# Performance work log

Hardware: AMD Instinct MI355X
Metric: run time of the kernel (lower is better)

Reference implementation:

```python
import jax, jax.numpy as jnp
import numpy as np


def setup_inputs() -> dict:
    key = jax.random.key(0)
    k1, k2 = jax.random.split(key)
    inputs = jax.random.normal(k1, (16, 64, 64, 512), dtype=jnp.float32)
    gamma = jax.random.normal(k2, (1,), dtype=jnp.float32)
    return {"inputs": inputs, "gamma": gamma}


def reference(inputs, gamma):
    # inputs: [B, H, W, C] (NHWC), gamma: [1]
    b, h, w, c = inputs.shape
    vec_a = inputs.reshape(b, h * w, c)           # [B, HW, C]
    # channel-channel Gram matrix: [B, C, C]
    aTa = jnp.einsum('bnc,bnd->bcd', vec_a, vec_a)
    softmax_aTa = jax.nn.softmax(aTa, axis=-1)     # softmax over last channel axis
    # attend over channels: [B, HW, C] @ [B, C, C] -> [B, HW, C]
    aaTa = jnp.einsum('bnc,bcd->bnd', vec_a, softmax_aTa)
    aaTa = aaTa.reshape(b, h, w, c)
    return gamma * aaTa + inputs
```

## Files before the change

kernel.cpp:

```cpp
#include <hip/hip_runtime.h>
#include <stdint.h>

#define BB 16
#define NN 4096
#define CC 512

typedef __attribute__((ext_vector_type(8))) short bf16x8;
typedef __attribute__((ext_vector_type(4))) float f32x4;

__device__ __forceinline__ unsigned short to_bf16(float f) {
  unsigned int u = __float_as_uint(f);
  u += 0x7fffu + ((u >> 16) & 1u);
  return (unsigned short)(u >> 16);
}

__device__ __forceinline__ void gload_lds16(const void* g, void* l) {
  __builtin_amdgcn_global_load_lds(
      (const __attribute__((address_space(1))) unsigned int*)g,
      (__attribute__((address_space(3))) unsigned int*)l, 16, 0, 0);
}

template <int KT>
__device__ __forceinline__ void nt_gemm(const unsigned short* __restrict__ aB,
                                        const unsigned short* __restrict__ bB,
                                        f32x4 acc[4][4],
                                        unsigned short* lA, unsigned short* lB) {
  const int tid  = threadIdx.x;
  const int wid  = tid >> 6;
  const int lane = tid & 63;
  const int wr   = (wid >> 1) * 64;
  const int wc   = (wid & 1) * 64;

  const f32x4 zero = {0.f, 0.f, 0.f, 0.f};
#pragma unroll
  for (int i = 0; i < 4; ++i)
#pragma unroll
    for (int j = 0; j < 4; ++j) acc[i][j] = zero;

  const int srow = lane >> 3;
  const int gsrc = (lane & 7) ^ srow;

#pragma unroll 1
  for (int k0 = 0; k0 < KT; k0 += 64) {
#pragma unroll
    for (int i = 0; i < 4; ++i) {
      const int issue = wid * 4 + i;
      const int row   = issue * 8 + srow;
      const size_t go = (size_t)row * KT + k0 + gsrc * 8;
      gload_lds16(aB + go, lA + issue * 512);
      gload_lds16(bB + go, lB + issue * 512);
    }
    __syncthreads();

#pragma unroll
    for (int s = 0; s < 2; ++s) {
      bf16x8 af[4], bfr[4];
#pragma unroll
      for (int mf = 0; mf < 4; ++mf) {
        const int row = wr + mf * 16 + (lane & 15);
        const int ch  = (s * 4 + (lane >> 4)) ^ (row & 7);
        af[mf] = *(const bf16x8*)(lA + row * 64 + ch * 8);
      }
#pragma unroll
      for (int nf = 0; nf < 4; ++nf) {
        const int row = wc + nf * 16 + (lane & 15);
        const int ch  = (s * 4 + (lane >> 4)) ^ (row & 7);
        bfr[nf] = *(const bf16x8*)(lB + row * 64 + ch * 8);
      }
#pragma unroll
      for (int mf = 0; mf < 4; ++mf)
#pragma unroll
        for (int nf = 0; nf < 4; ++nf)
          acc[mf][nf] = __builtin_amdgcn_mfma_f32_16x16x32_bf16(
              af[mf], bfr[nf], acc[mf][nf], 0, 0, 0);
    }
    __syncthreads();
  }
}

__global__ __launch_bounds__(256) void k_convert(const float* __restrict__ in,
                                                 unsigned short* __restrict__ a16,
                                                 unsigned short* __restrict__ at16) {
  __shared__ unsigned short lt[64][68];
  const int b  = blockIdx.y;
  const int tn = blockIdx.x >> 3, tc = blockIdx.x & 7;
  const int n0 = tn * 64, c0 = tc * 64;
  const float* src = in + ((size_t)b * NN + n0) * CC + c0;
  unsigned short* adst = a16 + ((size_t)b * NN + n0) * CC + c0;

#pragma unroll
  for (int i = 0; i < 4; ++i) {
    const int id = i * 256 + threadIdx.x;
    const int n = id >> 4, ch = id & 15;
    float4 v = *(const float4*)(src + (size_t)n * CC + ch * 4);
    ushort4 o;
    o.x = to_bf16(v.x); o.y = to_bf16(v.y); o.z = to_bf16(v.z); o.w = to_bf16(v.w);
    *(ushort4*)(adst + (size_t)n * CC + ch * 4) = o;
    lt[ch * 4 + 0][n] = o.x;
    lt[ch * 4 + 1][n] = o.y;
    lt[ch * 4 + 2][n] = o.z;
    lt[ch * 4 + 3][n] = o.w;
  }
  __syncthreads();
  unsigned short* tdst = at16 + ((size_t)b * CC + c0) * NN + n0;
#pragma unroll
  for (int i = 0; i < 4; ++i) {
    const int id = i * 256 + threadIdx.x;
    const int c = id >> 4, ch2 = id & 15;
    uint2 w = *(const uint2*)&lt[c][ch2 * 4];
    *(uint2*)(tdst + (size_t)c * NN + ch2 * 4) = w;
  }
}

__global__ __launch_bounds__(256) void k_gram(const unsigned short* __restrict__ at,
                                              float* __restrict__ gram) {
  __shared__ __align__(16) unsigned short lA[128 * 64];
  __shared__ __align__(16) unsigned short lB[128 * 64];
  const int b  = blockIdx.y;
  const int c0 = (blockIdx.x & 3) * 128;
  const int d0 = (blockIdx.x >> 2) * 128;
  const unsigned short* aB = at + ((size_t)b * CC + c0) * NN;
  const unsigned short* bB = at + ((size_t)b * CC + d0) * NN;
  f32x4 acc[4][4];
  nt_gemm<NN>(aB, bB, acc, lA, lB);

  const int lane = threadIdx.x & 63, wid = threadIdx.x >> 6;
  const int wr = (wid >> 1) * 64, wc = (wid & 1) * 64;
  float* gb = gram + (size_t)b * CC * CC;
#pragma unroll
  for (int mf = 0; mf < 4; ++mf)
#pragma unroll
    for (int nf = 0; nf < 4; ++nf)
#pragma unroll
      for (int r = 0; r < 4; ++r) {
        const int row = c0 + wr + mf * 16 + (lane >> 4) * 4 + r;
        const int col = d0 + wc + nf * 16 + (lane & 15);
        gb[(size_t)row * CC + col] = acc[mf][nf][r];
      }
}

__global__ __launch_bounds__(256) void k_rowstats(const float* __restrict__ gram,
                                                  float2* __restrict__ stats) {
  const int wid = threadIdx.x >> 6, lane = threadIdx.x & 63;
  const int row = blockIdx.x * 4 + wid;
  const float* src = gram + (size_t)row * CC;
  float4 v0 = *(const float4*)(src + lane * 4);
  float4 v1 = *(const float4*)(src + 256 + lane * 4);
  float m = fmaxf(fmaxf(fmaxf(v0.x, v0.y), fmaxf(v0.z, v0.w)),
                  fmaxf(fmaxf(v1.x, v1.y), fmaxf(v1.z, v1.w)));
#pragma unroll
  for (int off = 32; off > 0; off >>= 1) m = fmaxf(m, __shfl_xor(m, off));
  float s = expf(v0.x - m) + expf(v0.y - m) + expf(v0.z - m) + expf(v0.w - m) +
            expf(v1.x - m) + expf(v1.y - m) + expf(v1.z - m) + expf(v1.w - m);
#pragma unroll
  for (int off = 32; off > 0; off >>= 1) s += __shfl_xor(s, off);
  if (lane == 0) stats[row] = make_float2(m, 1.0f / s);
}

__global__ __launch_bounds__(256) void k_smax_t(const float* __restrict__ gram,
                                                const float2* __restrict__ stats,
                                                unsigned short* __restrict__ st) {
  __shared__ unsigned short lt[64][68];
  const int b  = blockIdx.y;
  const int c0 = (blockIdx.x >> 3) * 64, d0 = (blockIdx.x & 7) * 64;
  const float* gb = gram + ((size_t)b * CC + c0) * CC + d0;
  const float2* sb = stats + (size_t)b * CC + c0;
#pragma unroll
  for (int i = 0; i < 4; ++i) {
    const int id = i * 256 + threadIdx.x;
    const int c = id >> 4, ch = id & 15;
    const float2 stt = sb[c];
    float4 v = *(const float4*)(gb + (size_t)c * CC + ch * 4);
    float vv[4] = {v.x, v.y, v.z, v.w};
#pragma unroll
    for (int j = 0; j < 4; ++j)
      lt[ch * 4 + j][c] = to_bf16(expf(vv[j] - stt.x) * stt.y);
  }
  __syncthreads();
  unsigned short* ob = st + ((size_t)b * CC + d0) * CC + c0;
#pragma unroll
  for (int i = 0; i < 4; ++i) {
    const int id = i * 256 + threadIdx.x;
    const int d = id >> 4, ch2 = id & 15;
    uint2 w = *(const uint2*)&lt[d][ch2 * 4];
    *(uint2*)(ob + (size_t)d * CC + ch2 * 4) = w;
  }
}

__global__ __launch_bounds__(256) void k_out(const unsigned short* __restrict__ a16,
                                             const unsigned short* __restrict__ st,
                                             const float* __restrict__ x,
                                             const float* __restrict__ gammap,
                                             float* __restrict__ outp) {
  __shared__ __align__(16) unsigned short lA[128 * 64];
  __shared__ __align__(16) unsigned short lB[128 * 64];
  const int b  = blockIdx.y;
  const int mt = blockIdx.x >> 2, nt = blockIdx.x & 3;
  const int n0 = mt * 128, d0 = nt * 128;
  const unsigned short* aB = a16 + ((size_t)b * NN + n0) * CC;
  const unsigned short* bB = st + ((size_t)b * CC + d0) * CC;
  f32x4 acc[4][4];
  nt_gemm<CC>(aB, bB, acc, lA, lB);

  const float g = gammap[0];
  const int lane = threadIdx.x & 63, wid = threadIdx.x >> 6;
  const int wr = (wid >> 1) * 64, wc = (wid & 1) * 64;
  const float* xb = x + ((size_t)b * NN + n0) * CC + d0;
  float* ob = outp + ((size_t)b * NN + n0) * CC + d0;
#pragma unroll
  for (int mf = 0; mf < 4; ++mf)
#pragma unroll
    for (int nf = 0; nf < 4; ++nf)
#pragma unroll
      for (int r = 0; r < 4; ++r) {
        const int row = wr + mf * 16 + (lane >> 4) * 4 + r;
        const int col = wc + nf * 16 + (lane & 15);
        const size_t off = (size_t)row * CC + col;
        ob[off] = fmaf(g, acc[mf][nf][r], xb[off]);
      }
}

extern "C" void kernel_launch(void* const* d_in, const int* in_sizes, int n_in,
                              void* d_out, int out_size, void* d_ws, size_t ws_size,
                              hipStream_t stream) {
  const float* in    = (const float*)d_in[0];
  const float* gamma = (const float*)d_in[1];
  float* outp = (float*)d_out;

  unsigned short* a16  = (unsigned short*)d_ws;
  float*          gram = (float*)((char*)d_ws + ((size_t)64 << 20));
  unsigned short* st   = (unsigned short*)((char*)d_ws + ((size_t)80 << 20));
  float2*         stats = (float2*)((char*)d_ws + ((size_t)88 << 20));
  unsigned short* at16 = (unsigned short*)d_out;

  k_convert<<<dim3(512, 16), 256, 0, stream>>>(in, a16, at16);
  k_gram<<<dim3(16, 16), 256, 0, stream>>>(at16, gram);
  k_rowstats<<<dim3(2048), 256, 0, stream>>>(gram, stats);
  k_smax_t<<<dim3(64, 16), 256, 0, stream>>>(gram, stats, st);
  k_out<<<dim3(128, 16), 256, 0, stream>>>(a16, st, in, gamma, outp);
}
```

Measured before the change: 403.4 us.

## Split-K Gram GEMM, fuse softmax stages, swizzle block order, read residual as bf16

New measurement: 370.7 us. 8.1% less time.

```diff
diff --git a/kernel.cpp b/kernel.cpp
--- a/kernel.cpp
+++ b/kernel.cpp
@@ -4,6 +4,7 @@
 #define BB 16
 #define NN 4096
 #define CC 512
+#define PELEM ((size_t)BB * CC * CC)
 
 typedef __attribute__((ext_vector_type(8))) short bf16x8;
 typedef __attribute__((ext_vector_type(4))) float f32x4;
@@ -13,6 +14,9 @@
   u += 0x7fffu + ((u >> 16) & 1u);
   return (unsigned short)(u >> 16);
 }
+__device__ __forceinline__ float bf16_to_f32(unsigned short h) {
+  return __uint_as_float(((unsigned int)h) << 16);
+}
 
 __device__ __forceinline__ void gload_lds16(const void* g, void* l) {
   __builtin_amdgcn_global_load_lds(
@@ -20,7 +24,7 @@
       (__attribute__((address_space(3))) unsigned int*)l, 16, 0, 0);
 }
 
-template <int KT>
+template <int RS, int KLEN>
 __device__ __forceinline__ void nt_gemm(const unsigned short* __restrict__ aB,
                                         const unsigned short* __restrict__ bB,
                                         f32x4 acc[4][4],
@@ -41,12 +45,12 @@
   const int gsrc = (lane & 7) ^ srow;
 
 #pragma unroll 1
-  for (int k0 = 0; k0 < KT; k0 += 64) {
+  for (int k0 = 0; k0 < KLEN; k0 += 64) {
 #pragma unroll
     for (int i = 0; i < 4; ++i) {
       const int issue = wid * 4 + i;
       const int row   = issue * 8 + srow;
-      const size_t go = (size_t)row * KT + k0 + gsrc * 8;
+      const size_t go = (size_t)row * RS + k0 + gsrc * 8;
       gload_lds16(aB + go, lA + issue * 512);
       gload_lds16(bB + go, lB + issue * 512);
     }
@@ -113,110 +117,134 @@
 }
 
 __global__ __launch_bounds__(256) void k_gram(const unsigned short* __restrict__ at,
-                                              float* __restrict__ gram) {
+                                              float* __restrict__ parts) {
   __shared__ __align__(16) unsigned short lA[128 * 64];
   __shared__ __align__(16) unsigned short lB[128 * 64];
-  const int b  = blockIdx.y;
-  const int c0 = (blockIdx.x & 3) * 128;
-  const int d0 = (blockIdx.x >> 2) * 128;
-  const unsigned short* aB = at + ((size_t)b * CC + c0) * NN;
-  const unsigned short* bB = at + ((size_t)b * CC + d0) * NN;
+  const int bid  = blockIdx.x;
+  const int work = (bid & 7) * 128 + (bid >> 3);
+  const int b    = work >> 6;
+  const int r    = work & 63;
+  const int ks   = r >> 4;
+  const int tile = r & 15;
+  const int c0 = (tile & 3) * 128;
+  const int d0 = (tile >> 2) * 128;
+  const unsigned short* aB = at + ((size_t)b * CC + c0) * NN + ks * 1024;
+  const unsigned short* bB = at + ((size_t)b * CC + d0) * NN + ks * 1024;
   f32x4 acc[4][4];
-  nt_gemm<NN>(aB, bB, acc, lA, lB);
+  nt_gemm<NN, 1024>(aB, bB, acc, lA, lB);
 
   const int lane = threadIdx.x & 63, wid = threadIdx.x >> 6;
   const int wr = (wid >> 1) * 64, wc = (wid & 1) * 64;
-  float* gb = gram + (size_t)b * CC * CC;
+  float* gb = parts + (size_t)ks * PELEM + (size_t)b * CC * CC;
 #pragma unroll
   for (int mf = 0; mf < 4; ++mf)
 #pragma unroll
     for (int nf = 0; nf < 4; ++nf)
 #pragma unroll
-      for (int r = 0; r < 4; ++r) {
-        const int row = c0 + wr + mf * 16 + (lane >> 4) * 4 + r;
+      for (int q = 0; q < 4; ++q) {
+        const int row = c0 + wr + mf * 16 + (lane >> 4) * 4 + q;
         const int col = d0 + wc + nf * 16 + (lane & 15);
-        gb[(size_t)row * CC + col] = acc[mf][nf][r];
-      }
-}
-
-__global__ __launch_bounds__(256) void k_rowstats(const float* __restrict__ gram,
-                                                  float2* __restrict__ stats) {
+        gb[(size_t)row * CC + col] = acc[mf][nf][q];
+      }
+}
+
+__global__ __launch_bounds__(256) void k_softmax(const float* __restrict__ parts,
+                                                 unsigned short* __restrict__ st) {
+  __shared__ unsigned short ls[32][512];
+  const int b  = blockIdx.x >> 4;
+  const int cb = blockIdx.x & 15;
   const int wid = threadIdx.x >> 6, lane = threadIdx.x & 63;
-  const int row = blockIdx.x * 4 + wid;
-  const float* src = gram + (size_t)row * CC;
-  float4 v0 = *(const float4*)(src + lane * 4);
-  float4 v1 = *(const float4*)(src + 256 + lane * 4);
-  float m = fmaxf(fmaxf(fmaxf(v0.x, v0.y), fmaxf(v0.z, v0.w)),
-                  fmaxf(fmaxf(v1.x, v1.y), fmaxf(v1.z, v1.w)));
-#pragma unroll
-  for (int off = 32; off > 0; off >>= 1) m = fmaxf(m, __shfl_xor(m, off));
-  float s = expf(v0.x - m) + expf(v0.y - m) + expf(v0.z - m) + expf(v0.w - m) +
-            expf(v1.x - m) + expf(v1.y - m) + expf(v1.z - m) + expf(v1.w - m);
-#pragma unroll
-  for (int off = 32; off > 0; off >>= 1) s += __shfl_xor(s, off);
-  if (lane == 0) stats[row] = make_float2(m, 1.0f / s);
-}
-
-__global__ __launch_bounds__(256) void k_smax_t(const float* __restrict__ gram,
-                                                const float2* __restrict__ stats,
-                                                unsigned short* __restrict__ st) {
-  __shared__ unsigned short lt[64][68];
-  const int b  = blockIdx.y;
-  const int c0 = (blockIdx.x >> 3) * 64, d0 = (blockIdx.x & 7) * 64;
-  const float* gb = gram + ((size_t)b * CC + c0) * CC + d0;
-  const float2* sb = stats + (size_t)b * CC + c0;
-#pragma unroll
-  for (int i = 0; i < 4; ++i) {
-    const int id = i * 256 + threadIdx.x;
-    const int c = id >> 4, ch = id & 15;
-    const float2 stt = sb[c];
-    float4 v = *(const float4*)(gb + (size_t)c * CC + ch * 4);
-    float vv[4] = {v.x, v.y, v.z, v.w};
-#pragma unroll
-    for (int j = 0; j < 4; ++j)
-      lt[ch * 4 + j][c] = to_bf16(expf(vv[j] - stt.x) * stt.y);
+
+#pragma unroll 1
+  for (int i = 0; i < 8; ++i) {
+    const int rl = wid * 8 + i;
+    const int c  = cb * 32 + rl;
+    const int r7 = rl & 7;
+    const float* base = parts + ((size_t)b * CC + c) * CC;
+    float4 v0 = {0.f, 0.f, 0.f, 0.f}, v1 = {0.f, 0.f, 0.f, 0.f};
+#pragma unroll
+    for (int p = 0; p < 4; ++p) {
+      float4 a = *(const float4*)(base + (size_t)p * PELEM + lane * 4);
+      float4 bq = *(const float4*)(base + (size_t)p * PELEM + 256 + lane * 4);
+      v0.x += a.x; v0.y += a.y; v0.z += a.z; v0.w += a.w;
+      v1.x += bq.x; v1.y += bq.y; v1.z += bq.z; v1.w += bq.w;
+    }
+    float m = fmaxf(fmaxf(fmaxf(v0.x, v0.y), fmaxf(v0.z, v0.w)),
+                    fmaxf(fmaxf(v1.x, v1.y), fmaxf(v1.z, v1.w)));
+#pragma unroll
+    for (int off = 32; off > 0; off >>= 1) m = fmaxf(m, __shfl_xor(m, off));
+    float e0 = expf(v0.x - m), e1 = expf(v0.y - m), e2 = expf(v0.z - m), e3 = expf(v0.w - m);
+    float e4 = expf(v1.x - m), e5 = expf(v1.y - m), e6 = expf(v1.z - m), e7 = expf(v1.w - m);
+    float s = e0 + e1 + e2 + e3 + e4 + e5 + e6 + e7;
+#pragma unroll
+    for (int off = 32; off > 0; off >>= 1) s += __shfl_xor(s, off);
+    const float pinv = 1.0f / s;
+    ushort4 o0, o1;
+    o0.x = to_bf16(e0 * pinv); o0.y = to_bf16(e1 * pinv);
+    o0.z = to_bf16(e2 * pinv); o0.w = to_bf16(e3 * pinv);
+    o1.x = to_bf16(e4 * pinv); o1.y = to_bf16(e5 * pinv);
+    o1.z = to_bf16(e6 * pinv); o1.w = to_bf16(e7 * pinv);
+    *(ushort4*)&ls[rl][(lane ^ r7) << 2]         = o0;
+    *(ushort4*)&ls[rl][256 + ((lane ^ r7) << 2)] = o1;
   }
   __syncthreads();
-  unsigned short* ob = st + ((size_t)b * CC + d0) * CC + c0;
-#pragma unroll
-  for (int i = 0; i < 4; ++i) {
-    const int id = i * 256 + threadIdx.x;
-    const int d = id >> 4, ch2 = id & 15;
-    uint2 w = *(const uint2*)&lt[d][ch2 * 4];
-    *(uint2*)(ob + (size_t)d * CC + ch2 * 4) = w;
+
+#pragma unroll 1
+  for (int i = 0; i < 2; ++i) {
+    const int d = i * 256 + threadIdx.x;
+    unsigned int u[16];
+#pragma unroll
+    for (int k = 0; k < 16; ++k) {
+      const int c0i = 2 * k, c1i = 2 * k + 1;
+      const unsigned int lo = ls[c0i][(((d >> 2) ^ (c0i & 7)) << 2) | (d & 3)];
+      const unsigned int hi = ls[c1i][(((d >> 2) ^ (c1i & 7)) << 2) | (d & 3)];
+      u[k] = lo | (hi << 16);
+    }
+    unsigned short* dst = st + ((size_t)b * CC + d) * CC + cb * 32;
+    uint4 w0 = {u[0], u[1], u[2], u[3]};
+    uint4 w1 = {u[4], u[5], u[6], u[7]};
+    uint4 w2 = {u[8], u[9], u[10], u[11]};
+    uint4 w3 = {u[12], u[13], u[14], u[15]};
+    *(uint4*)(dst + 0)  = w0;
+    *(uint4*)(dst + 8)  = w1;
+    *(uint4*)(dst + 16) = w2;
+    *(uint4*)(dst + 24) = w3;
   }
 }
 
 __global__ __launch_bounds__(256) void k_out(const unsigned short* __restrict__ a16,
                                              const unsigned short* __restrict__ st,
-                                             const float* __restrict__ x,
                                              const float* __restrict__ gammap,
                                              float* __restrict__ outp) {
   __shared__ __align__(16) unsigned short lA[128 * 64];
   __shared__ __align__(16) unsigned short lB[128 * 64];
-  const int b  = blockIdx.y;
-  const int mt = blockIdx.x >> 2, nt = blockIdx.x & 3;
+  const int bid  = blockIdx.x;
+  const int work = (bid & 7) * 256 + (bid >> 3);
+  const int b    = work >> 7;
+  const int r    = work & 127;
+  const int nt   = r >> 5;
+  const int mt   = r & 31;
   const int n0 = mt * 128, d0 = nt * 128;
   const unsigned short* aB = a16 + ((size_t)b * NN + n0) * CC;
   const unsigned short* bB = st + ((size_t)b * CC + d0) * CC;
   f32x4 acc[4][4];
-  nt_gemm<CC>(aB, bB, acc, lA, lB);
+  nt_gemm<CC, CC>(aB, bB, acc, lA, lB);
 
   const float g = gammap[0];
   const int lane = threadIdx.x & 63, wid = threadIdx.x >> 6;
   const int wr = (wid >> 1) * 64, wc = (wid & 1) * 64;
-  const float* xb = x + ((size_t)b * NN + n0) * CC + d0;
+  const unsigned short* xr = a16 + ((size_t)b * NN + n0) * CC + d0;
   float* ob = outp + ((size_t)b * NN + n0) * CC + d0;
 #pragma unroll
   for (int mf = 0; mf < 4; ++mf)
 #pragma unroll
     for (int nf = 0; nf < 4; ++nf)
 #pragma unroll
-      for (int r = 0; r < 4; ++r) {
-        const int row = wr + mf * 16 + (lane >> 4) * 4 + r;
+      for (int q = 0; q < 4; ++q) {
+        const int row = wr + mf * 16 + (lane >> 4) * 4 + q;
         const int col = wc + nf * 16 + (lane & 15);
         const size_t off = (size_t)row * CC + col;
-        ob[off] = fmaf(g, acc[mf][nf][r], xb[off]);
+        ob[off] = fmaf(g, acc[mf][nf][q], bf16_to_f32(xr[off]));
       }
 }
 
@@ -228,14 +256,12 @@
   float* outp = (float*)d_out;
 
   unsigned short* a16  = (unsigned short*)d_ws;
-  float*          gram = (float*)((char*)d_ws + ((size_t)64 << 20));
-  unsigned short* st   = (unsigned short*)((char*)d_ws + ((size_t)80 << 20));
-  float2*         stats = (float2*)((char*)d_ws + ((size_t)88 << 20));
+  unsigned short* stb  = (unsigned short*)((char*)d_ws + ((size_t)64 << 20));
   unsigned short* at16 = (unsigned short*)d_out;
+  float*          parts = (float*)((char*)d_out + ((size_t)64 << 20));
 
   k_convert<<<dim3(512, 16), 256, 0, stream>>>(in, a16, at16);
-  k_gram<<<dim3(16, 16), 256, 0, stream>>>(at16, gram);
-  k_rowstats<<<dim3(2048), 256, 0, stream>>>(gram, stats);
-  k_smax_t<<<dim3(64, 16), 256, 0, stream>>>(gram, stats, st);
-  k_out<<<dim3(128, 16), 256, 0, stream>>>(a16, st, in, gamma, outp);
-}
+  k_gram<<<dim3(1024), 256, 0, stream>>>(at16, parts);
+  k_softmax<<<dim3(256), 256, 0, stream>>>(parts, stb);
+  k_out<<<dim3(2048), 256, 0, stream>>>(a16, stb, gamma, outp);
+}
```
